# Optimization experiments

Measured on AMD Instinct MI355X. Metric: run time of the kernel, lower is better.

Reference implementation:

```python
import jax, jax.numpy as jnp
import numpy as np

GAMMA = 1.0   # focal exponent
THETA = 1.0   # boundary weight scale
SIGMA = 1.0   # distance decay
EPS = 1e-8
BIG = 1e10    # 'no boundary point in this column' sentinel


def _boundary(mask):
    # mask: [H,W] bool. Boundary = foreground pixel with a 4-neighbor background
    # (image border counts as background via zero padding).
    p = jnp.pad(mask, 1)
    inner = (p[1:-1, 1:-1] & p[:-2, 1:-1] & p[2:, 1:-1]
             & p[1:-1, :-2] & p[1:-1, 2:])
    return mask & ~inner


def _sqdist(mask):
    # Exact squared Euclidean distance transform to the True pixels of mask,
    # via separable two-pass min:  d2(x,y) = min_{y'} [ (y-y')^2 + min_{x':mask[x',y']} (x-x')^2 ]
    H, W = mask.shape
    xs = jnp.arange(H, dtype=jnp.float32)
    dx2 = (xs[:, None] - xs[None, :]) ** 2                      # [H,H]
    col = jnp.where(mask, 0.0, BIG)                             # [H,W]
    g = jnp.min(dx2[:, :, None] + col[None, :, :], axis=1)      # [H,W] min over x'
    ys = jnp.arange(W, dtype=jnp.float32)
    dy2 = (ys[:, None] - ys[None, :]) ** 2                      # [W,W] (y,y')
    return jnp.min(g[:, None, :] + dy2[None, :, :], axis=2)     # [H,W] min over y'


def _weight_map(prob, label):
    # prob, label: [H,W] float
    ib = _boundary(prob > 0.5)    # predicted-image boundary pixels
    lb = _boundary(label > 0.5)   # label boundary pixels
    d_to_ib = jnp.sqrt(_sqdist(ib))   # distance of every pixel to nearest image boundary
    d_to_lb = jnp.sqrt(_sqdist(lb))   # distance of every pixel to nearest label boundary
    w = (1.0
         + THETA * jnp.where(lb, jnp.exp(-d_to_ib / SIGMA), 0.0)
         + THETA * jnp.where(ib, jnp.exp(-d_to_lb / SIGMA), 0.0))
    return w


def setup_inputs() -> dict:
    key = jax.random.key(0)
    k1, k2 = jax.random.split(key)
    B, H, W = 8, 256, 256
    inp = jax.random.normal(k1, (B, H, W), dtype=jnp.float32)
    target = (jax.random.uniform(k2, (B, H, W)) < 0.5).astype(jnp.float32)
    return {"input": inp, "target": target}


def reference(input, target):
    probs = jax.nn.sigmoid(input)
    # weight maps are built from detached CPU copies in the original -> stop_gradient
    w = jax.lax.stop_gradient(jax.vmap(_weight_map)(probs, target))
    loss = w * (-(1.0 - probs) ** GAMMA * target * jnp.log(probs + EPS)
                - probs ** GAMMA * (1.0 - target) * jnp.log(1.0 - probs + EPS))
    return jnp.mean(loss)
```

## Files before the change

### kernel.cpp

```cpp
#include <hip/hip_runtime.h>

#define HW_BIG   1e10f
#define LOSS_EPS 1e-8f

typedef unsigned long long u64;

__device__ __forceinline__ int row_nearest(const u64* rm, int y) {
    const int yw = y >> 6, yb = y & 63;
    int dd = 32768;
    u64 w = rm[yw] & (~0ULL >> (63 - yb));
    int j = yw;
    while (w == 0 && j > 0) w = rm[--j];
    if (w) dd = y - (j * 64 + 63 - __builtin_clzll(w));
    u64 w2 = rm[yw] & (~0ULL << yb);
    int j2 = yw;
    while (w2 == 0 && j2 < 3) w2 = rm[++j2];
    if (w2) { int du = (j2 * 64 + __builtin_ctzll(w2)) - y; dd = min(dd, du); }
    return dd;
}

__global__ void k_masks(const float* __restrict__ inp,
                        const float* __restrict__ tgt,
                        u64* __restrict__ rows_bib,
                        u64* __restrict__ rows_blb,
                        u64* __restrict__ rows_ml) {
    __shared__ u64 V[6][4];
    __shared__ u64 T[6][4];
    const int tid = threadIdx.x;
    const int img = blockIdx.x >> 6;
    const int r0  = (blockIdx.x & 63) * 4;
    const int r   = tid >> 8;
    const int y   = tid & 255;
    const int w   = y >> 6;
    const float* ip = inp + (size_t)img * 65536;
    const float* tp = tgt + (size_t)img * 65536;

    const int x = r0 + r;
    bool vb = ip[x * 256 + y] > 0.0f;
    bool tb = tp[x * 256 + y] > 0.5f;
    u64 bv = __ballot(vb);
    u64 bt = __ballot(tb);
    if ((y & 63) == 0) { V[r][w] = bv; T[r][w] = bt; }

    if (tid < 256) {
        const int xh = r0 - 1;
        bool hv = (xh >= 0) && (ip[xh * 256 + y] > 0.0f);
        bool ht = (xh >= 0) && (tp[xh * 256 + y] > 0.5f);
        u64 a = __ballot(hv), b = __ballot(ht);
        if ((y & 63) == 0) { V[4][w] = a; T[4][w] = b; }
    } else if (tid < 512) {
        const int xh = r0 + 4;
        bool hv = (xh < 256) && (ip[xh * 256 + y] > 0.0f);
        bool ht = (xh < 256) && (tp[xh * 256 + y] > 0.5f);
        u64 a = __ballot(hv), b = __ballot(ht);
        if ((y & 63) == 0) { V[5][w] = a; T[5][w] = b; }
    }
    __syncthreads();

    if (tid < 32) {
        const int rr = (tid >> 2) & 3;
        const int j  = tid & 3;
        const bool isT = tid >= 16;
        const u64 (*M)[4] = isT ? T : V;
        u64 own = M[rr][j];
        u64 up  = (rr == 0) ? M[4][j] : M[rr - 1][j];
        u64 dn  = (rr == 3) ? M[5][j] : M[rr + 1][j];
        u64 lf  = (own << 1) | ((j > 0) ? (M[rr][j - 1] >> 63) : 0ULL);
        u64 rt  = (own >> 1) | ((j < 3) ? (M[rr][j + 1] << 63) : 0ULL);
        u64 bnd = own & ~(up & dn & lf & rt);
        const size_t o = ((size_t)img * 256 + (r0 + rr)) * 4 + j;
        if (!isT) rows_bib[o] = bnd;
        else      { rows_blb[o] = bnd; rows_ml[o] = own; }
    }
}

__global__ void k_dt_loss(const float* __restrict__ inp,
                          const u64* __restrict__ rows_bib,
                          const u64* __restrict__ rows_blb,
                          const u64* __restrict__ rows_ml,
                          float* __restrict__ partials) {
    __shared__ u64 Mib[1024];
    __shared__ u64 Mlb[1024];
    __shared__ u64 Mml[1024];
    __shared__ float G1[4][256];
    __shared__ float G2[4][256];
    __shared__ float wsum[16];
    const int tid = threadIdx.x;
    const int img = blockIdx.x >> 6;
    const int y0  = (blockIdx.x & 63) * 4;
    const int yr  = tid >> 8;
    const int x   = tid & 255;
    const int y   = y0 + yr;
    const int yw  = y >> 6, yb = y & 63;

    const size_t mbase = (size_t)img * 1024;
    Mib[tid] = rows_bib[mbase + tid];
    Mlb[tid] = rows_blb[mbase + tid];
    Mml[tid] = rows_ml[mbase + tid];
    const float v = inp[((size_t)img * 256 + x) * 256 + y];
    __syncthreads();

    const bool fib = (Mib[x * 4 + yw] >> yb) & 1;
    const bool flb = (Mlb[x * 4 + yw] >> yb) & 1;
    const float t  = ((Mml[x * 4 + yw] >> yb) & 1) ? 1.0f : 0.0f;

    const int d1 = row_nearest(&Mib[x * 4], y);
    const int d2 = row_nearest(&Mlb[x * 4], y);
    G1[yr][x] = (d1 > 255) ? HW_BIG : (float)(d1 * d1);
    G2[yr][x] = (d2 > 255) ? HW_BIG : (float)(d2 * d2);
    __syncthreads();

    float m1 = flb ? G1[yr][x] : 0.0f;
    float m2 = fib ? G2[yr][x] : 0.0f;
    for (int d = 1; d < 256; ++d) {
        const float fd2 = (float)(d * d);
        if (fd2 >= m1 && fd2 >= m2) break;
        const int xl = x - d;
        if (xl >= 0)  { m1 = fminf(m1, G1[yr][xl] + fd2); m2 = fminf(m2, G2[yr][xl] + fd2); }
        const int xr = x + d;
        if (xr < 256) { m1 = fminf(m1, G1[yr][xr] + fd2); m2 = fminf(m2, G2[yr][xr] + fd2); }
    }

    const float p = 1.0f / (1.0f + expf(-v));
    float wgt = 1.0f;
    if (flb) wgt += expf(-sqrtf(m1));
    if (fib) wgt += expf(-sqrtf(m2));

    float loss = wgt * (-(1.0f - p) * t * logf(p + LOSS_EPS)
                        - p * (1.0f - t) * logf(1.0f - p + LOSS_EPS));

    float s = loss;
#pragma unroll
    for (int off = 32; off > 0; off >>= 1) s += __shfl_down(s, off, 64);
    if ((tid & 63) == 0) wsum[tid >> 6] = s;
    __syncthreads();
    if (tid == 0) {
        float bs = 0.0f;
#pragma unroll
        for (int i = 0; i < 16; ++i) bs += wsum[i];
        partials[blockIdx.x] = bs;
    }
}

__global__ void k_reduce(const float* __restrict__ partials, int n,
                         float* __restrict__ out, double inv_count) {
    __shared__ double sw[4];
    const int tid = threadIdx.x;
    double s = 0.0;
    for (int i = tid; i < n; i += 256) s += (double)partials[i];
#pragma unroll
    for (int off = 32; off > 0; off >>= 1) s += __shfl_down(s, off, 64);
    const int lane = tid & 63, wv = tid >> 6;
    if (lane == 0) sw[wv] = s;
    __syncthreads();
    if (tid == 0) out[0] = (float)(((sw[0] + sw[1]) + (sw[2] + sw[3])) * inv_count);
}

extern "C" void kernel_launch(void* const* d_in, const int* in_sizes, int n_in,
                              void* d_out, int out_size, void* d_ws, size_t ws_size,
                              hipStream_t stream) {
    const float* inp = (const float*)d_in[0];
    const float* tgt = (const float*)d_in[1];
    float* out = (float*)d_out;

    const int total = in_sizes[0];
    const int nimg  = total / 65536;
    const int nblk  = nimg * 64;

    char* ws = (char*)d_ws;
    u64*   rows_bib = (u64*)ws;
    u64*   rows_blb = rows_bib + (size_t)nimg * 1024;
    u64*   rows_ml  = rows_blb + (size_t)nimg * 1024;
    float* parts    = (float*)(rows_ml + (size_t)nimg * 1024);

    k_masks  <<<nblk, 1024, 0, stream>>>(inp, tgt, rows_bib, rows_blb, rows_ml);
    k_dt_loss<<<nblk, 1024, 0, stream>>>(inp, rows_bib, rows_blb, rows_ml, parts);
    k_reduce <<<1,    256,  0, stream>>>(parts, nblk, out, 1.0 / (double)total);
}
```

Before: 18.90 us.

## Remap threads x-major in distance kernel and fold reduction into atomics

The thread-to-pixel mapping in the distance/loss kernel changes so that consecutive threads cover the 4 columns of the same row, and the shared G arrays become [256][4]. The intent is coalesced global reads of the input, since v is read at x*256+y. The third reduce kernel is removed: each block atomically adds its scaled partial sum to the output, which the mask kernel zeroes first. This saves one launch at the cost of a non-deterministic float summation order, and it changes the lane pattern of the shared-memory accesses.

```diff
diff --git a/kernel.cpp b/kernel.cpp
--- a/kernel.cpp
+++ b/kernel.cpp
@@ -23,7 +23,8 @@
                         const float* __restrict__ tgt,
                         u64* __restrict__ rows_bib,
                         u64* __restrict__ rows_blb,
-                        u64* __restrict__ rows_ml) {
+                        u64* __restrict__ rows_ml,
+                        float* __restrict__ out) {
     __shared__ u64 V[6][4];
     __shared__ u64 T[6][4];
     const int tid = threadIdx.x;
@@ -34,6 +35,8 @@
     const int w   = y >> 6;
     const float* ip = inp + (size_t)img * 65536;
     const float* tp = tgt + (size_t)img * 65536;
+
+    if (blockIdx.x == 0 && tid == 0) out[0] = 0.0f;
 
     const int x = r0 + r;
     bool vb = ip[x * 256 + y] > 0.0f;
@@ -78,18 +81,19 @@
                           const u64* __restrict__ rows_bib,
                           const u64* __restrict__ rows_blb,
                           const u64* __restrict__ rows_ml,
-                          float* __restrict__ partials) {
+                          float* __restrict__ out,
+                          float inv_count) {
     __shared__ u64 Mib[1024];
     __shared__ u64 Mlb[1024];
     __shared__ u64 Mml[1024];
-    __shared__ float G1[4][256];
-    __shared__ float G2[4][256];
+    __shared__ float G1[256][4];
+    __shared__ float G2[256][4];
     __shared__ float wsum[16];
     const int tid = threadIdx.x;
     const int img = blockIdx.x >> 6;
     const int y0  = (blockIdx.x & 63) * 4;
-    const int yr  = tid >> 8;
-    const int x   = tid & 255;
+    const int x   = tid >> 2;
+    const int yr  = tid & 3;
     const int y   = y0 + yr;
     const int yw  = y >> 6, yb = y & 63;
 
@@ -106,19 +110,19 @@
 
     const int d1 = row_nearest(&Mib[x * 4], y);
     const int d2 = row_nearest(&Mlb[x * 4], y);
-    G1[yr][x] = (d1 > 255) ? HW_BIG : (float)(d1 * d1);
-    G2[yr][x] = (d2 > 255) ? HW_BIG : (float)(d2 * d2);
+    G1[x][yr] = (d1 > 255) ? HW_BIG : (float)(d1 * d1);
+    G2[x][yr] = (d2 > 255) ? HW_BIG : (float)(d2 * d2);
     __syncthreads();
 
-    float m1 = flb ? G1[yr][x] : 0.0f;
-    float m2 = fib ? G2[yr][x] : 0.0f;
+    float m1 = flb ? G1[x][yr] : 0.0f;
+    float m2 = fib ? G2[x][yr] : 0.0f;
     for (int d = 1; d < 256; ++d) {
         const float fd2 = (float)(d * d);
         if (fd2 >= m1 && fd2 >= m2) break;
         const int xl = x - d;
-        if (xl >= 0)  { m1 = fminf(m1, G1[yr][xl] + fd2); m2 = fminf(m2, G2[yr][xl] + fd2); }
+        if (xl >= 0)  { m1 = fminf(m1, G1[xl][yr] + fd2); m2 = fminf(m2, G2[xl][yr] + fd2); }
         const int xr = x + d;
-        if (xr < 256) { m1 = fminf(m1, G1[yr][xr] + fd2); m2 = fminf(m2, G2[yr][xr] + fd2); }
+        if (xr < 256) { m1 = fminf(m1, G1[xr][yr] + fd2); m2 = fminf(m2, G2[xr][yr] + fd2); }
     }
 
     const float p = 1.0f / (1.0f + expf(-v));
@@ -138,22 +142,8 @@
         float bs = 0.0f;
 #pragma unroll
         for (int i = 0; i < 16; ++i) bs += wsum[i];
-        partials[blockIdx.x] = bs;
+        atomicAdd(out, bs * inv_count);
     }
-}
-
-__global__ void k_reduce(const float* __restrict__ partials, int n,
-                         float* __restrict__ out, double inv_count) {
-    __shared__ double sw[4];
-    const int tid = threadIdx.x;
-    double s = 0.0;
-    for (int i = tid; i < n; i += 256) s += (double)partials[i];
-#pragma unroll
-    for (int off = 32; off > 0; off >>= 1) s += __shfl_down(s, off, 64);
-    const int lane = tid & 63, wv = tid >> 6;
-    if (lane == 0) sw[wv] = s;
-    __syncthreads();
-    if (tid == 0) out[0] = (float)(((sw[0] + sw[1]) + (sw[2] + sw[3])) * inv_count);
 }
 
 extern "C" void kernel_launch(void* const* d_in, const int* in_sizes, int n_in,
@@ -168,12 +158,11 @@
     const int nblk  = nimg * 64;
 
     char* ws = (char*)d_ws;
-    u64*   rows_bib = (u64*)ws;
-    u64*   rows_blb = rows_bib + (size_t)nimg * 1024;
-    u64*   rows_ml  = rows_blb + (size_t)nimg * 1024;
-    float* parts    = (float*)(rows_ml + (size_t)nimg * 1024);
+    u64* rows_bib = (u64*)ws;
+    u64* rows_blb = rows_bib + (size_t)nimg * 1024;
+    u64* rows_ml  = rows_blb + (size_t)nimg * 1024;
 
-    k_masks  <<<nblk, 1024, 0, stream>>>(inp, tgt, rows_bib, rows_blb, rows_ml);
-    k_dt_loss<<<nblk, 1024, 0, stream>>>(inp, rows_bib, rows_blb, rows_ml, parts);
-    k_reduce <<<1,    256,  0, stream>>>(parts, nblk, out, 1.0 / (double)total);
+    k_masks  <<<nblk, 1024, 0, stream>>>(inp, tgt, rows_bib, rows_blb, rows_ml, out);
+    k_dt_loss<<<nblk, 1024, 0, stream>>>(inp, rows_bib, rows_blb, rows_ml, out,
+                                         1.0f / (float)total);
 }
```

Result: slower. 20.18 us (+6.8%).

## Process eight columns per block, two per thread, with transposed distance tables

Applied to the files above, without the earlier changes.

The distance-transform and loss kernel now covers 8 y-columns per block instead of 4, halving the block count and how often each block reloads the per-image mask rows into shared memory. Each thread handles two y positions, and the G tables become [x][8] so the 4 adjacent threads of an x share nearby shared-memory addresses. Fast __expf and __logf intrinsics replace expf and logf. The cost is fewer blocks (256) for the GPU, more serial work per thread from two early-exit scan loops, and strided input reads along y.

```diff
diff --git a/kernel.cpp b/kernel.cpp
--- a/kernel.cpp
+++ b/kernel.cpp
@@ -82,54 +82,82 @@
     __shared__ u64 Mib[1024];
     __shared__ u64 Mlb[1024];
     __shared__ u64 Mml[1024];
-    __shared__ float G1[4][256];
-    __shared__ float G2[4][256];
+    __shared__ float G1[256][8];
+    __shared__ float G2[256][8];
     __shared__ float wsum[16];
     const int tid = threadIdx.x;
-    const int img = blockIdx.x >> 6;
-    const int y0  = (blockIdx.x & 63) * 4;
-    const int yr  = tid >> 8;
-    const int x   = tid & 255;
-    const int y   = y0 + yr;
-    const int yw  = y >> 6, yb = y & 63;
+    const int img = blockIdx.x >> 5;
+    const int y0  = (blockIdx.x & 31) * 8;
+    const int x   = tid >> 2;
+    const int yq  = tid & 3;
+    const int ya  = y0 + yq;
+    const int yb  = ya + 4;
 
     const size_t mbase = (size_t)img * 1024;
     Mib[tid] = rows_bib[mbase + tid];
     Mlb[tid] = rows_blb[mbase + tid];
     Mml[tid] = rows_ml[mbase + tid];
-    const float v = inp[((size_t)img * 256 + x) * 256 + y];
-    __syncthreads();
-
-    const bool fib = (Mib[x * 4 + yw] >> yb) & 1;
-    const bool flb = (Mlb[x * 4 + yw] >> yb) & 1;
-    const float t  = ((Mml[x * 4 + yw] >> yb) & 1) ? 1.0f : 0.0f;
-
-    const int d1 = row_nearest(&Mib[x * 4], y);
-    const int d2 = row_nearest(&Mlb[x * 4], y);
-    G1[yr][x] = (d1 > 255) ? HW_BIG : (float)(d1 * d1);
-    G2[yr][x] = (d2 > 255) ? HW_BIG : (float)(d2 * d2);
-    __syncthreads();
-
-    float m1 = flb ? G1[yr][x] : 0.0f;
-    float m2 = fib ? G2[yr][x] : 0.0f;
+    const float va = inp[((size_t)img * 256 + x) * 256 + ya];
+    const float vb = inp[((size_t)img * 256 + x) * 256 + yb];
+    __syncthreads();
+
+    const int ywa = ya >> 6, yba = ya & 63;
+    const int ywb = yb >> 6, ybb = yb & 63;
+    const bool fibA = (Mib[x * 4 + ywa] >> yba) & 1;
+    const bool flbA = (Mlb[x * 4 + ywa] >> yba) & 1;
+    const float tA  = ((Mml[x * 4 + ywa] >> yba) & 1) ? 1.0f : 0.0f;
+    const bool fibB = (Mib[x * 4 + ywb] >> ybb) & 1;
+    const bool flbB = (Mlb[x * 4 + ywb] >> ybb) & 1;
+    const float tB  = ((Mml[x * 4 + ywb] >> ybb) & 1) ? 1.0f : 0.0f;
+
+    {
+        const int d1a = row_nearest(&Mib[x * 4], ya);
+        const int d2a = row_nearest(&Mlb[x * 4], ya);
+        const int d1b = row_nearest(&Mib[x * 4], yb);
+        const int d2b = row_nearest(&Mlb[x * 4], yb);
+        G1[x][yq]     = (d1a > 255) ? HW_BIG : (float)(d1a * d1a);
+        G2[x][yq]     = (d2a > 255) ? HW_BIG : (float)(d2a * d2a);
+        G1[x][yq + 4] = (d1b > 255) ? HW_BIG : (float)(d1b * d1b);
+        G2[x][yq + 4] = (d2b > 255) ? HW_BIG : (float)(d2b * d2b);
+    }
+    __syncthreads();
+
+    float m1a = flbA ? G1[x][yq] : 0.0f;
+    float m2a = fibA ? G2[x][yq] : 0.0f;
     for (int d = 1; d < 256; ++d) {
         const float fd2 = (float)(d * d);
-        if (fd2 >= m1 && fd2 >= m2) break;
+        if (fd2 >= m1a && fd2 >= m2a) break;
         const int xl = x - d;
-        if (xl >= 0)  { m1 = fminf(m1, G1[yr][xl] + fd2); m2 = fminf(m2, G2[yr][xl] + fd2); }
+        if (xl >= 0)  { m1a = fminf(m1a, G1[xl][yq] + fd2); m2a = fminf(m2a, G2[xl][yq] + fd2); }
         const int xr = x + d;
-        if (xr < 256) { m1 = fminf(m1, G1[yr][xr] + fd2); m2 = fminf(m2, G2[yr][xr] + fd2); }
-    }
-
-    const float p = 1.0f / (1.0f + expf(-v));
-    float wgt = 1.0f;
-    if (flb) wgt += expf(-sqrtf(m1));
-    if (fib) wgt += expf(-sqrtf(m2));
-
-    float loss = wgt * (-(1.0f - p) * t * logf(p + LOSS_EPS)
-                        - p * (1.0f - t) * logf(1.0f - p + LOSS_EPS));
-
-    float s = loss;
+        if (xr < 256) { m1a = fminf(m1a, G1[xr][yq] + fd2); m2a = fminf(m2a, G2[xr][yq] + fd2); }
+    }
+    float m1b = flbB ? G1[x][yq + 4] : 0.0f;
+    float m2b = fibB ? G2[x][yq + 4] : 0.0f;
+    for (int d = 1; d < 256; ++d) {
+        const float fd2 = (float)(d * d);
+        if (fd2 >= m1b && fd2 >= m2b) break;
+        const int xl = x - d;
+        if (xl >= 0)  { m1b = fminf(m1b, G1[xl][yq + 4] + fd2); m2b = fminf(m2b, G2[xl][yq + 4] + fd2); }
+        const int xr = x + d;
+        if (xr < 256) { m1b = fminf(m1b, G1[xr][yq + 4] + fd2); m2b = fminf(m2b, G2[xr][yq + 4] + fd2); }
+    }
+
+    const float pa = 1.0f / (1.0f + __expf(-va));
+    float wA = 1.0f;
+    if (flbA) wA += __expf(-sqrtf(m1a));
+    if (fibA) wA += __expf(-sqrtf(m2a));
+    float lossA = wA * (-(1.0f - pa) * tA * __logf(pa + LOSS_EPS)
+                        - pa * (1.0f - tA) * __logf(1.0f - pa + LOSS_EPS));
+
+    const float pb = 1.0f / (1.0f + __expf(-vb));
+    float wB = 1.0f;
+    if (flbB) wB += __expf(-sqrtf(m1b));
+    if (fibB) wB += __expf(-sqrtf(m2b));
+    float lossB = wB * (-(1.0f - pb) * tB * __logf(pb + LOSS_EPS)
+                        - pb * (1.0f - tB) * __logf(1.0f - pb + LOSS_EPS));
+
+    float s = lossA + lossB;
 #pragma unroll
     for (int off = 32; off > 0; off >>= 1) s += __shfl_down(s, off, 64);
     if ((tid & 63) == 0) wsum[tid >> 6] = s;
@@ -165,7 +193,8 @@
 
     const int total = in_sizes[0];
     const int nimg  = total / 65536;
-    const int nblk  = nimg * 64;
+    const int nblk1 = nimg * 64;
+    const int nblk2 = nimg * 32;
 
     char* ws = (char*)d_ws;
     u64*   rows_bib = (u64*)ws;
@@ -173,7 +202,7 @@
     u64*   rows_ml  = rows_blb + (size_t)nimg * 1024;
     float* parts    = (float*)(rows_ml + (size_t)nimg * 1024);
 
-    k_masks  <<<nblk, 1024, 0, stream>>>(inp, tgt, rows_bib, rows_blb, rows_ml);
-    k_dt_loss<<<nblk, 1024, 0, stream>>>(inp, rows_bib, rows_blb, rows_ml, parts);
-    k_reduce <<<1,    256,  0, stream>>>(parts, nblk, out, 1.0 / (double)total);
-}
+    k_masks  <<<nblk1, 1024, 0, stream>>>(inp, tgt, rows_bib, rows_blb, rows_ml);
+    k_dt_loss<<<nblk2, 1024, 0, stream>>>(inp, rows_bib, rows_blb, rows_ml, parts);
+    k_reduce <<<1,     256,  0, stream>>>(parts, nblk2, out, 1.0 / (double)total);
+}
```

Result: faster. 17.23 us (-8.8%).
